# Performance work log

Hardware: AMD Instinct MI355X
Metric: run time of the kernel (lower is better)

Reference implementation:

```python
import jax, jax.numpy as jnp
import numpy as np

B, S, D, H = 2, 2048, 1024, 16
DK = D // H  # 64


def setup_inputs() -> dict:
    key = jax.random.key(0)
    ks = jax.random.split(key, 4)
    scale = 1.0 / np.sqrt(D)
    return {
        "q_input": jax.random.normal(ks[0], (B, S, D), dtype=jnp.float32),
        "W_q": jax.random.normal(ks[1], (D, D), dtype=jnp.float32) * scale,
        "b_q": jnp.zeros((D,), dtype=jnp.float32),
        "W_k": jax.random.normal(ks[2], (D, D), dtype=jnp.float32) * scale,
        "b_k": jnp.zeros((D,), dtype=jnp.float32),
        "W_v": jax.random.normal(ks[3], (D, D), dtype=jnp.float32) * scale,
        "b_v": jnp.zeros((D,), dtype=jnp.float32),
    }


def reference(q_input, W_q, b_q, W_k, b_k, W_v, b_v):
    # Self-attention: k_input and v_input default to q_input in the torch module.
    # nn.Linear computes x @ W.T + b
    q = q_input @ W_q.T + b_q
    k = q_input @ W_k.T + b_k
    v = q_input @ W_v.T + b_v

    # [B,S,D] -> [B,H,S,DK]
    def split_heads(x):
        return x.reshape(B, S, H, DK).transpose(0, 2, 1, 3)

    qh, kh, vh = split_heads(q), split_heads(k), split_heads(v)

    # scores [B,H,S,S]; causal mask added BEFORE scaling (as in source; -inf invariant)
    scores = jnp.einsum("bhqd,bhkd->bhqk", qh, kh)
    causal = jnp.tril(jnp.ones((S, S), dtype=bool))
    scores = jnp.where(causal[None, None], scores, -jnp.inf)
    scores = scores / jnp.sqrt(jnp.float32(DK))
    probs = jax.nn.softmax(scores, axis=-1)
    z = jnp.einsum("bhqk,bhkd->bhqd", probs, vh)  # [B,H,S,DK]
    # [B,H,S,DK] -> [B,S,H,DK] -> [B,S,D]
    return z.transpose(0, 2, 1, 3).reshape(B, S, D)
```

## Files before the change

kernel.cpp:

```cpp
#include <hip/hip_runtime.h>
#include <hip/hip_bf16.h>
#include <stdint.h>

typedef __attribute__((ext_vector_type(8))) short short8;
typedef __attribute__((ext_vector_type(4))) short short4v;
typedef __attribute__((ext_vector_type(4))) float f32x4;
typedef __attribute__((ext_vector_type(16))) float f32x16;

#define B_ 2
#define S_ 2048
#define D_ 1024
#define H_ 16
#define DK_ 64
#define M_ (B_*S_)

#define WS_QKV   0
#define WS_XB    12582912
#define WS_WB    16777216

#define QSCALE (0.125f * 1.44269504088896f)

#define GLL16(g, l) __builtin_amdgcn_global_load_lds( \
    (const __attribute__((address_space(1))) void*)(g), \
    (__attribute__((address_space(3))) void*)(l), 16, 0, 0)

#define WAIT_VM0 asm volatile("s_waitcnt vmcnt(0)" ::: "memory")
#define WAIT_VM4 asm volatile("s_waitcnt vmcnt(4)" ::: "memory")
#define WAIT_VM8 asm volatile("s_waitcnt vmcnt(8)" ::: "memory")
#define WAIT_LGKM0 asm volatile("s_waitcnt lgkmcnt(0)" ::: "memory")
#define BARRIER_RAW asm volatile("s_barrier" ::: "memory")

static __device__ __forceinline__ short f2bf(float f){
  union { float f; unsigned u; } x; x.f = f;
  unsigned r = x.u + 0x7fff + ((x.u >> 16) & 1);
  return (short)(r >> 16);
}

__global__ __launch_bounds__(256) void cvt_bf16(
    const float* __restrict__ X,  const float* __restrict__ Wq,
    const float* __restrict__ Wk, const float* __restrict__ Wv,
    short* __restrict__ ws)
{
  const int z = blockIdx.z;
  const float* src; short* dst; int n;
  if (z == 0)      { src = X;  dst = ws + WS_XB;               n = M_*D_; }
  else if (z == 1) { src = Wq; dst = ws + WS_WB;               n = D_*D_; }
  else if (z == 2) { src = Wk; dst = ws + WS_WB + D_*D_;       n = D_*D_; }
  else             { src = Wv; dst = ws + WS_WB + 2*(D_*D_);   n = D_*D_; }
  const int stride = gridDim.x * blockDim.x * 4;
  for (int i = (blockIdx.x * blockDim.x + threadIdx.x) * 4; i < n; i += stride) {
    float4 v = *(const float4*)(src + i);
    short4v o;
    o.x = f2bf(v.x); o.y = f2bf(v.y); o.z = f2bf(v.z); o.w = f2bf(v.w);
    *(short4v*)(dst + i) = o;
  }
}

__global__ __launch_bounds__(512, 2) void qkv_gemm(
    const short* __restrict__ ws_in,
    const float* __restrict__ bq, const float* __restrict__ bk,
    const float* __restrict__ bv, short* __restrict__ qkv)
{
  const int z = blockIdx.z;
  const short* X  = ws_in + WS_XB;
  const short* Wm = ws_in + WS_WB + (size_t)z * (D_*D_);
  short* out = qkv + (size_t)z * (M_*D_);

  __shared__ __align__(16) short lds[65536];

  const int t = threadIdx.x;
  const int w = t >> 6, lane = t & 63;
  const int quad = lane >> 4, l16 = lane & 15;
  const int wm = w >> 2, wn = w & 3;
  const int m0 = blockIdx.y * 256, n0 = blockIdx.x * 256;

  const int rl = t >> 2;
  const int sl = (t & 3) ^ (rl & 3);
  const short* sA0 = X  + (size_t)(m0 + rl) * D_ + sl*8;
  const short* sA1 = sA0 + (size_t)128 * D_;
  const short* sB0 = Wm + (size_t)(n0 + rl) * D_ + sl*8;
  const short* sB1 = sB0 + (size_t)128 * D_;
  const int ldsw = w << 9;

  const int swz = quad ^ (l16 & 3);

  f32x4 acc[8][4];
  #pragma unroll
  for (int i=0;i<8;i++)
    #pragma unroll
    for (int j=0;j<4;j++) acc[i][j] = (f32x4){0.f,0.f,0.f,0.f};

  #pragma unroll
  for (int p=0;p<3;p++){
    GLL16(sA0 + p*32, lds + p*16384 + ldsw);
    GLL16(sA1 + p*32, lds + p*16384 + 4096 + ldsw);
    GLL16(sB0 + p*32, lds + p*16384 + 8192 + ldsw);
    GLL16(sB1 + p*32, lds + p*16384 + 12288 + ldsw);
  }
  WAIT_VM8;
  BARRIER_RAW;

  for (int kt = 0; kt < 32; kt++) {
    const int bf = kt & 3;
    const short* bufA = lds + bf*16384;
    const short* bufB = bufA + 8192;
    const int tb = (kt + 3) & 3;
    const int ko2 = (kt + 3) * 32;

    if (kt + 3 < 32) {
      GLL16(sA0 + ko2, lds + tb*16384 + ldsw);
      GLL16(sA1 + ko2, lds + tb*16384 + 4096 + ldsw);
      GLL16(sB0 + ko2, lds + tb*16384 + 8192 + ldsw);
      GLL16(sB1 + ko2, lds + tb*16384 + 12288 + ldsw);
    }

    short8 bF[4], aF[8];
    #pragma unroll
    for (int nf=0; nf<4; nf++)
      bF[nf] = *(const short8*)(bufB + (wn*64 + nf*16 + l16)*32 + swz*8);
    #pragma unroll
    for (int mf=0; mf<8; mf++)
      aF[mf] = *(const short8*)(bufA + (wm*128 + mf*16 + l16)*32 + swz*8);

    __builtin_amdgcn_s_setprio(1);
    #pragma unroll
    for (int mf=0; mf<8; mf++)
      #pragma unroll
      for (int nf=0; nf<4; nf++)
        acc[mf][nf] = __builtin_amdgcn_mfma_f32_16x16x32_bf16(aF[mf], bF[nf], acc[mf][nf], 0,0,0);
    __builtin_amdgcn_s_setprio(0);

    if      (kt < 29)  { WAIT_VM8; }
    else if (kt == 29) { WAIT_VM4; }
    else if (kt == 30) { WAIT_VM0; }
    BARRIER_RAW;
  }

  __syncthreads();

  if (z != 2) {
    const float scale = (z==0) ? QSCALE : 1.0f;
    const float* bias = (z==0) ? bq : bk;
    float bv4[4];
    #pragma unroll
    for (int nf=0; nf<4; nf++) bv4[nf] = bias[n0 + wn*64 + nf*16 + l16];
    short* ep = lds;
    #pragma unroll
    for (int p=0; p<2; p++){
      if (wm == p){
        #pragma unroll
        for (int mf=0; mf<8; mf++)
          #pragma unroll
          for (int nf=0; nf<4; nf++)
            #pragma unroll
            for (int i=0; i<4; i++)
              ep[(mf*16 + quad*4 + i)*264 + wn*64 + nf*16 + l16] =
                  f2bf((acc[mf][nf][i] + bv4[nf]) * scale);
      }
      __syncthreads();
      #pragma unroll
      for (int it=0; it<8; it++){
        const int cid = it*512 + t;
        const int row = cid >> 5, cc = cid & 31;
        short8 vv = *(const short8*)(ep + row*264 + cc*8);
        const int m = m0 + p*128 + row, bidx = m >> 11, s = m & 2047;
        const int n = n0 + cc*8, h = n >> 6, dd = n & 63;
        *(short8*)(out + (((size_t)(bidx*H_ + h))*S_ + s)*DK_ + dd) = vv;
      }
      __syncthreads();
    }
  } else {
    float bv4[4];
    #pragma unroll
    for (int nf=0; nf<4; nf++) bv4[nf] = bv[n0 + wn*64 + nf*16 + l16];
    short* ep = lds;
    #pragma unroll
    for (int p=0; p<2; p++){
      if (wm == p){
        #pragma unroll
        for (int mf=0; mf<8; mf++)
          #pragma unroll
          for (int nf=0; nf<4; nf++)
            #pragma unroll
            for (int i=0; i<4; i++)
              ep[(wn*64 + nf*16 + l16)*136 + mf*16 + quad*4 + i] =
                  f2bf(acc[mf][nf][i] + bv4[nf]);
      }
      __syncthreads();
      #pragma unroll
      for (int it=0; it<8; it++){
        const int cid = it*512 + t;
        const int row = cid >> 4, cc = cid & 15;
        short8 vv = *(const short8*)(ep + row*136 + cc*8);
        const int n = n0 + row, h = n >> 6, dd = n & 63;
        const int m0p = m0 + p*128;
        const int bidx = m0p >> 11;
        const int s = (m0p & 2047) + cc*8;
        *(short8*)(out + (((size_t)(bidx*H_ + h))*DK_ + dd)*S_ + s) = vv;
      }
      __syncthreads();
    }
  }
}

static __device__ __forceinline__ void attn_steps(
    const int nSteps, const int I0, const int nA, const int q0w,
    const short8* __restrict__ bqv,
    const short* __restrict__ K, const short* __restrict__ VT,
    short (*Kbuf)[4096], short (*Vbuf)[4096],
    const int g, const int w, const int l32, const int h, const int xrow,
    const int row0, const int sc8,
    f32x16& o0, f32x16& o1, float& lsum)
{
  for (int j = 0; j < nSteps; ++j){
    const int I  = I0 + j;
    const int gt = 2*I + g;
    const int kb = (2*j + g)*64;
    const bool active = (kb <= q0w + 31);
    const short* Kc = &Kbuf[gt & 3][0];
    const short* Vc = &Vbuf[gt & 3][0];

    short8 ak[8], vk[8];
    if (active){
      #pragma unroll
      for (int dc=0; dc<4; dc++){
        const int xk = ((dc*2 + h) ^ xrow)*8;
        ak[dc]   = *(const short8*)(Kc + l32*64 + xk);
        ak[4+dc] = *(const short8*)(Kc + (32 + l32)*64 + xk);
        vk[dc]   = *(const short8*)(Vc + l32*64 + xk);
        vk[4+dc] = *(const short8*)(Vc + (32 + l32)*64 + xk);
      }
    }
    WAIT_LGKM0;
    BARRIER_RAW;

    #pragma unroll
    for (int q=0; q<2; q++){
      const int gp = 2*I + 4 + q;
      if (gp < 34){
        const int kbp = (gp < nA ? gp : gp - nA) * 64;
        GLL16(K  + (size_t)(kbp + row0)*DK_ + sc8, &Kbuf[gp & 3][0] + w*512);
        GLL16(VT + (size_t)row0*S_ + kbp + sc8,    &Vbuf[gp & 3][0] + w*512);
      }
    }

    if (active){
      f32x16 s[2];
      #pragma unroll
      for (int e=0;e<16;e++){ s[0][e] = 0.f; s[1][e] = 0.f; }
      #pragma unroll
      for (int dc=0; dc<4; dc++){
        s[0] = __builtin_amdgcn_mfma_f32_32x32x16_bf16(ak[dc],   bqv[dc], s[0], 0,0,0);
        s[1] = __builtin_amdgcn_mfma_f32_32x32x16_bf16(ak[4+dc], bqv[dc], s[1], 0,0,0);
      }

      if (kb + 63 > q0w) {
        const int qg = q0w + l32;
        #pragma unroll
        for (int r=0; r<16; r++){
          const int k0 = kb + (r&3) + 8*(r>>2) + 4*h;
          if (k0      > qg) s[0][r] = -3.0e38f;
          if (k0 + 32 > qg) s[1][r] = -3.0e38f;
        }
      }

      short8 pf[4];
      #pragma unroll
      for (int mk=0; mk<2; mk++){
        #pragma unroll
        for (int u=0; u<2; u++){
          float p0 = __builtin_amdgcn_exp2f(s[mk][8*u+0]);
          float p1 = __builtin_amdgcn_exp2f(s[mk][8*u+1]);
          float p2 = __builtin_amdgcn_exp2f(s[mk][8*u+2]);
          float p3 = __builtin_amdgcn_exp2f(s[mk][8*u+3]);
          float p4 = __builtin_amdgcn_exp2f(s[mk][8*u+4]);
          float p5 = __builtin_amdgcn_exp2f(s[mk][8*u+5]);
          float p6 = __builtin_amdgcn_exp2f(s[mk][8*u+6]);
          float p7 = __builtin_amdgcn_exp2f(s[mk][8*u+7]);
          lsum += ((p0+p1)+(p2+p3)) + ((p4+p5)+(p6+p7));
          unsigned X0, X1, Y0, Y1;
          asm("v_cvt_pk_bf16_f32 %0, %1, %2" : "=v"(X0) : "v"(p0), "v"(p1));
          asm("v_cvt_pk_bf16_f32 %0, %1, %2" : "=v"(X1) : "v"(p2), "v"(p3));
          asm("v_cvt_pk_bf16_f32 %0, %1, %2" : "=v"(Y0) : "v"(p4), "v"(p5));
          asm("v_cvt_pk_bf16_f32 %0, %1, %2" : "=v"(Y1) : "v"(p6), "v"(p7));
          asm("v_permlane32_swap_b32 %0, %1" : "+v"(X0), "+v"(Y0));
          asm("v_permlane32_swap_b32 %0, %1" : "+v"(X1), "+v"(Y1));
          union { unsigned u4[4]; short8 s8; } pp;
          pp.u4[0] = X0; pp.u4[1] = X1; pp.u4[2] = Y0; pp.u4[3] = Y1;
          pf[mk*2 + u] = pp.s8;
        }
      }

      #pragma unroll
      for (int kk=0; kk<4; kk++){
        o0 = __builtin_amdgcn_mfma_f32_32x32x16_bf16(pf[kk], vk[kk],   o0, 0,0,0);
        o1 = __builtin_amdgcn_mfma_f32_32x32x16_bf16(pf[kk], vk[4+kk], o1, 0,0,0);
      }
    }

    if      (I < 15)  { WAIT_VM4; }
    else if (I == 15) { WAIT_VM0; }
    if (I < 16) BARRIER_RAW;
  }
}

static __device__ __forceinline__ void attn_merge_store(
    float* __restrict__ out, const int bb, const int hh, const int qbase,
    const int w, const int wq, const int lane, const int l32, const int h,
    f32x16& o0, f32x16& o1, float& lsum,
    float (*ms)[64][33])
{
  if (w >= 4){
    #pragma unroll
    for (int e=0; e<16; e++){
      ms[wq][lane][e]    = o0[e];
      ms[wq][lane][16+e] = o1[e];
    }
    ms[wq][lane][32] = lsum;
  }
  WAIT_LGKM0;
  BARRIER_RAW;
  if (w < 4){
    #pragma unroll
    for (int e=0; e<16; e++){
      o0[e] += ms[wq][lane][e];
      o1[e] += ms[wq][lane][16+e];
    }
    float ls = lsum + ms[wq][lane][32];
    float rs = ls + __shfl_xor(ls, 32, 64);
    float linv = 1.0f / rs;
    #pragma unroll
    for (int r=0; r<16; r++){
      const int qrow = (r&3) + 8*(r>>2) + 4*h;
      const float lw = __shfl(linv, qrow, 64);
      float* dst = out + ((size_t)bb*S_ + (qbase + qrow))*D_ + hh*DK_;
      dst[l32]      = o0[r] * lw;
      dst[32 + l32] = o1[r] * lw;
    }
  }
  #pragma unroll
  for (int e=0; e<16; e++){ o0[e] = 0.f; o1[e] = 0.f; }
  lsum = 0.f;
}

__global__ __launch_bounds__(512, 1) void attn(
    const short* __restrict__ qkv, float* __restrict__ out)
{
  const int id = blockIdx.x;
  const int slot = id >> 3;
  const int bh = (id & 7) + 8*(slot & 3);
  const int p  = slot >> 2;
  const int nA = 2*p + 2;

  const short* Q  = qkv + (size_t)bh * (S_*DK_);
  const short* K  = Q + (size_t)(M_*D_);
  const short* VT = qkv + (size_t)(2*M_*D_) + (size_t)bh * (DK_*S_);

  __shared__ short Kbuf[4][4096];
  __shared__ short Vbuf[4][4096];
  __shared__ float ms[4][64][33];

  const int t = threadIdx.x;
  const int w = t >> 6, lane = t & 63;
  const int g = w >> 2, wq = w & 3;
  const int l32 = lane & 31, h = lane >> 5;
  const int xrow = l32 & 7;

  const int qA0 = p*128 + wq*32;
  const int qB0 = (15-p)*128 + wq*32;

  short8 bqA[4], bqB[4];
  #pragma unroll
  for (int dc=0; dc<4; dc++){
    bqA[dc] = *(const short8*)(Q + (size_t)(qA0 + l32)*DK_ + dc*16 + h*8);
    bqB[dc] = *(const short8*)(Q + (size_t)(qB0 + l32)*DK_ + dc*16 + h*8);
  }
  #pragma unroll
  for (int dc=0; dc<4; dc++){
    asm volatile("" : "+v"(bqA[dc]));
    asm volatile("" : "+v"(bqB[dc]));
  }

  const int r8   = lane >> 3;
  const int sc8  = ((lane & 7) ^ r8) * 8;
  const int row0 = w*8 + r8;

  #pragma unroll
  for (int pt=0; pt<4; pt++){
    const int kb = (pt < nA ? pt : pt - nA) * 64;
    GLL16(K  + (size_t)(kb + row0)*DK_ + sc8, &Kbuf[pt][0] + w*512);
    GLL16(VT + (size_t)row0*S_ + kb + sc8,    &Vbuf[pt][0] + w*512);
  }
  WAIT_VM4;
  BARRIER_RAW;

  f32x16 o0, o1;
  #pragma unroll
  for (int e=0; e<16; e++){ o0[e] = 0.f; o1[e] = 0.f; }
  float lsum = 0.f;
  const int bb = bh >> 4, hh = bh & 15;

  attn_steps(nA/2, 0, nA, qA0, bqA, K, VT, Kbuf, Vbuf,
             g, w, l32, h, xrow, row0, sc8, o0, o1, lsum);
  attn_merge_store(out, bb, hh, qA0, w, wq, lane, l32, h, o0, o1, lsum, ms);

  attn_steps(17 - nA/2, nA/2, nA, qB0, bqB, K, VT, Kbuf, Vbuf,
             g, w, l32, h, xrow, row0, sc8, o0, o1, lsum);
  attn_merge_store(out, bb, hh, qB0, w, wq, lane, l32, h, o0, o1, lsum, ms);
}

extern "C" void kernel_launch(void* const* d_in, const int* in_sizes, int n_in,
                              void* d_out, int out_size, void* d_ws, size_t ws_size,
                              hipStream_t stream)
{
  (void)in_sizes; (void)n_in; (void)out_size; (void)ws_size;
  const float* X  = (const float*)d_in[0];
  const float* Wq = (const float*)d_in[1];
  const float* bq = (const float*)d_in[2];
  const float* Wk = (const float*)d_in[3];
  const float* bk = (const float*)d_in[4];
  const float* Wv = (const float*)d_in[5];
  const float* bv = (const float*)d_in[6];
  short* ws  = (short*)d_ws;
  float* out = (float*)d_out;

  dim3 g0(1024, 1, 4);
  cvt_bf16<<<g0, dim3(256,1,1), 0, stream>>>(X, Wq, Wk, Wv, ws);
  dim3 g1(D_/256, M_/256, 3);
  qkv_gemm<<<g1, dim3(512,1,1), 0, stream>>>(ws, bq, bk, bv, ws + WS_QKV);
  dim3 g2(256, 1);
  attn<<<g2, dim3(512,1,1), 0, stream>>>(ws + WS_QKV, out);
}
```

Before: 160.2 us.

## Double-buffer LDS fragments in registers and deepen QKV GEMM prefetch

The QKV projection GEMM main loop now loads the next k-step's A/B fragments from LDS into a second register set while the MFMAs for the current step run, so LDS read latency is hidden behind compute. The global-to-LDS prefetch depth rises from 3 to 4 stages, with the recycled buffer being the one just consumed, and the vmcnt wait thresholds are shifted to match. This costs extra VGPRs for the second fragment set, which could lower occupancy or cause spills, and the buffer-reuse ordering relies on the barriers being placed correctly.

```diff
diff --git a/kernel.cpp b/kernel.cpp
--- a/kernel.cpp
+++ b/kernel.cpp
@@ -84,6 +84,12 @@
 
   const int swz = quad ^ (l16 & 3);
 
+  int aoff[8], boff[4];
+  #pragma unroll
+  for (int mf=0; mf<8; mf++) aoff[mf] = (wm*128 + mf*16 + l16)*32 + swz*8;
+  #pragma unroll
+  for (int nf=0; nf<4; nf++) boff[nf] = (wn*64 + nf*16 + l16)*32 + swz*8;
+
   f32x4 acc[8][4];
   #pragma unroll
   for (int i=0;i<8;i++)
@@ -91,7 +97,7 @@
     for (int j=0;j<4;j++) acc[i][j] = (f32x4){0.f,0.f,0.f,0.f};
 
   #pragma unroll
-  for (int p=0;p<3;p++){
+  for (int p=0;p<4;p++){
     GLL16(sA0 + p*32, lds + p*16384 + ldsw);
     GLL16(sA1 + p*32, lds + p*16384 + 4096 + ldsw);
     GLL16(sB0 + p*32, lds + p*16384 + 8192 + ldsw);
@@ -100,41 +106,54 @@
   WAIT_VM8;
   BARRIER_RAW;
 
-  for (int kt = 0; kt < 32; kt++) {
-    const int bf = kt & 3;
-    const short* bufA = lds + bf*16384;
-    const short* bufB = bufA + 8192;
-    const int tb = (kt + 3) & 3;
-    const int ko2 = (kt + 3) * 32;
-
-    if (kt + 3 < 32) {
-      GLL16(sA0 + ko2, lds + tb*16384 + ldsw);
-      GLL16(sA1 + ko2, lds + tb*16384 + 4096 + ldsw);
-      GLL16(sB0 + ko2, lds + tb*16384 + 8192 + ldsw);
-      GLL16(sB1 + ko2, lds + tb*16384 + 12288 + ldsw);
-    }
-
-    short8 bF[4], aF[8];
-    #pragma unroll
-    for (int nf=0; nf<4; nf++)
-      bF[nf] = *(const short8*)(bufB + (wn*64 + nf*16 + l16)*32 + swz*8);
-    #pragma unroll
-    for (int mf=0; mf<8; mf++)
-      aF[mf] = *(const short8*)(bufA + (wm*128 + mf*16 + l16)*32 + swz*8);
-
-    __builtin_amdgcn_s_setprio(1);
-    #pragma unroll
-    for (int mf=0; mf<8; mf++)
-      #pragma unroll
-      for (int nf=0; nf<4; nf++)
-        acc[mf][nf] = __builtin_amdgcn_mfma_f32_16x16x32_bf16(aF[mf], bF[nf], acc[mf][nf], 0,0,0);
-    __builtin_amdgcn_s_setprio(0);
-
-    if      (kt < 29)  { WAIT_VM8; }
-    else if (kt == 29) { WAIT_VM4; }
-    else if (kt == 30) { WAIT_VM0; }
-    BARRIER_RAW;
-  }
+  short8 F0[12], F1[12];
+  #pragma unroll
+  for (int nf=0; nf<4; nf++) F0[8+nf] = *(const short8*)(lds + 8192 + boff[nf]);
+  #pragma unroll
+  for (int mf=0; mf<8; mf++) F0[mf]   = *(const short8*)(lds + aoff[mf]);
+  WAIT_LGKM0;
+  BARRIER_RAW;
+
+#define QKV_WINDOW(KT, CUR, NXT)                                           \
+  {                                                                        \
+    const int kt_ = (KT);                                                  \
+    if (kt_ + 1 < 32){                                                     \
+      const short* nb = lds + ((kt_+1)&3)*16384;                           \
+      _Pragma("unroll")                                                    \
+      for (int nf=0; nf<4; nf++)                                           \
+        NXT[8+nf] = *(const short8*)(nb + 8192 + boff[nf]);                \
+      _Pragma("unroll")                                                    \
+      for (int mf=0; mf<8; mf++)                                           \
+        NXT[mf] = *(const short8*)(nb + aoff[mf]);                         \
+    }                                                                      \
+    if (kt_ + 4 < 32){                                                     \
+      const int ko = (kt_+4)*32;                                           \
+      short* tb = lds + (kt_&3)*16384;                                     \
+      GLL16(sA0 + ko, tb + ldsw);                                          \
+      GLL16(sA1 + ko, tb + 4096 + ldsw);                                   \
+      GLL16(sB0 + ko, tb + 8192 + ldsw);                                   \
+      GLL16(sB1 + ko, tb + 12288 + ldsw);                                  \
+    }                                                                      \
+    __builtin_amdgcn_s_setprio(1);                                         \
+    _Pragma("unroll")                                                      \
+    for (int mf=0; mf<8; mf++)                                             \
+      _Pragma("unroll")                                                    \
+      for (int nf=0; nf<4; nf++)                                           \
+        acc[mf][nf] = __builtin_amdgcn_mfma_f32_16x16x32_bf16(             \
+            CUR[mf], CUR[8+nf], acc[mf][nf], 0,0,0);                       \
+    __builtin_amdgcn_s_setprio(0);                                         \
+    WAIT_LGKM0;                                                            \
+    if      (kt_ <= 27) { WAIT_VM8; }                                      \
+    else if (kt_ == 28) { WAIT_VM4; }                                      \
+    else if (kt_ == 29) { WAIT_VM0; }                                      \
+    if (kt_ < 31) BARRIER_RAW;                                             \
+  }
+
+  for (int kt = 0; kt < 32; kt += 2){
+    QKV_WINDOW(kt,     F0, F1);
+    QKV_WINDOW(kt + 1, F1, F0);
+  }
+#undef QKV_WINDOW
 
   __syncthreads();
 
```

Result: no change. 157.8 us (-1.5%).
